# Kernel optimization log

Hardware: AMD Instinct MI355X
Metric: run time of the kernel (lower is better)

Reference implementation:

```python
import jax, jax.numpy as jnp
import numpy as np

EPS = 1e-4

def safe_clamp(x, max_val):
    # nan -> 0, +inf -> max_val, -inf -> -max_val, then clamp to [-max_val, max_val]
    x = jnp.where(jnp.isnan(x), 0.0, x)
    x = jnp.where(jnp.isinf(x) & (x > 0), max_val, x)
    x = jnp.where(jnp.isinf(x) & (x < 0), -max_val, x)
    return jnp.clip(x, -max_val, max_val)

def setup_inputs() -> dict:
    key = jax.random.key(0)
    k1, k2 = jax.random.split(key)
    hidden_states = jax.random.normal(k1, (4, 4096, 2048), dtype=jnp.float32)
    ln_weight = jnp.ones((2048,), dtype=jnp.float32)
    ln_bias = jnp.zeros((2048,), dtype=jnp.float32)
    gate_weight = jax.random.normal(k2, (64, 2048), dtype=jnp.float32) * 0.01
    return {"hidden_states": hidden_states, "ln_weight": ln_weight,
            "ln_bias": ln_bias, "gate_weight": gate_weight}

def reference(hidden_states, ln_weight, ln_bias, gate_weight):
    B, S, H = hidden_states.shape
    top_k = 2
    x = hidden_states.reshape(-1, H)  # (N, H)
    # LayerNorm(eps=1e-5)
    mu = jnp.mean(x, axis=-1, keepdims=True)
    var = jnp.mean((x - mu) ** 2, axis=-1, keepdims=True)
    x = (x - mu) * jax.lax.rsqrt(var + 1e-5) * ln_weight + ln_bias
    x = safe_clamp(x, 50.0)
    # gate: (N, H) @ (H, E)
    router_logits = jnp.clip(x @ gate_weight.T, -10.0, 10.0)
    # eval mode: no noise
    router_probs = jnp.clip(jax.nn.softmax(router_logits, axis=-1), EPS, 1.0)
    top_k_probs, top_k_indices = jax.lax.top_k(router_probs, top_k)
    prob_sum = jnp.maximum(jnp.sum(top_k_probs, axis=-1, keepdims=True), EPS)
    top_k_probs = top_k_probs / prob_sum
    return top_k_probs, top_k_indices, router_logits
```

## Files before the change

### kernel.cpp

```cpp
#include <hip/hip_runtime.h>
#include <math.h>

#define H 2048
#define E 64
#define MR 16
#define NCH 16
#define LR 136

typedef _Float16 half8  __attribute__((ext_vector_type(8)));
typedef _Float16 half4h __attribute__((ext_vector_type(4)));
typedef float    f32x4  __attribute__((ext_vector_type(4)));

#define MFMA16(A,B,C) __builtin_amdgcn_mfma_f32_16x16x32_f16(A,B,C,0,0,0)


__global__ __launch_bounds__(256) void prep_fused(const float* __restrict__ W,
        const float* __restrict__ lnw, const float* __restrict__ lnb,
        _Float16* __restrict__ Bh, _Float16* __restrict__ Bl,
        float* __restrict__ csum, float* __restrict__ bsum) {
    {
        int idx  = blockIdx.x * 256 + threadIdx.x;
        int lane = idx & 63;
        int e  = ((idx >> 6) & 3) * 16 + (lane & 15);
        int k0 = (idx >> 8) * 32 + ((lane >> 4) << 3);
        half8 hh, ll;
        #pragma unroll
        for (int j = 0; j < 8; ++j) {
            float wf = lnw[k0 + j] * W[e * H + k0 + j];
            _Float16 h = (_Float16)wf;
            _Float16 l = (_Float16)((wf - (float)h) * 2048.0f);
            hh[j] = h; ll[j] = l;
        }
        *(half8*)&Bh[(long)idx * 8] = hh;
        *(half8*)&Bl[(long)idx * 8] = ll;
    }
    {
        __shared__ float rc[256], rb[256];
        int e = blockIdx.x, t = threadIdx.x;
        float cs = 0.f, bs = 0.f;
        #pragma unroll
        for (int j = 0; j < 8; ++j) {
            int k = t + j * 256;
            float w = W[e * H + k];
            cs += lnw[k] * w;
            bs += lnb[k] * w;
        }
        rc[t] = cs; rb[t] = bs;
        __syncthreads();
        for (int s = 128; s > 0; s >>= 1) {
            if (t < s) { rc[t] += rc[t + s]; rb[t] += rb[t + s]; }
            __syncthreads();
        }
        if (t == 0) { csum[e] = rc[0]; bsum[e] = rb[0]; }
    }
}

__global__ __launch_bounds__(256, 4) void router_kernel(
    const float* __restrict__ X, const _Float16* __restrict__ Bh,
    const _Float16* __restrict__ Bl, const float* __restrict__ csum,
    const float* __restrict__ bsum, float* __restrict__ out, int nRows)
{
    __shared__ __align__(16) _Float16 Xh[2][MR][LR];
    __shared__ __align__(16) _Float16 Xl[2][MR][LR];
    __shared__ float C2[MR][E + 4];
    __shared__ float mu_s[MR], rs_s[MR];

    const int t    = threadIdx.x;
    const int lane = t & 63;
    const int et   = t >> 6;
    const int q    = lane >> 4;
    const int ln16 = lane & 15;
    const int rowR = t >> 4;
    const int cS   = t & 15;
    const long rowBase = (long)blockIdx.x * MR;
    const long iOff = (long)nRows * 2;
    const long lOff = (long)nRows * 4;

    const float4* Xrow = (const float4*)X + (rowBase + rowR) * 512;

    float sacc = 0.f, qacc = 0.f;

    f32x4 acc0 = (f32x4)0.f;
    f32x4 acc1 = (f32x4)0.f;

    auto convert = [&](const float4* vb, int buf) {
        #pragma unroll
        for (int j = 0; j < 2; ++j) {
            float4 v = vb[j];
            sacc += v.x + v.y + v.z + v.w;
            qacc += v.x * v.x + v.y * v.y + v.z * v.z + v.w * v.w;
            _Float16 h0 = (_Float16)v.x, h1 = (_Float16)v.y,
                     h2 = (_Float16)v.z, h3 = (_Float16)v.w;
            _Float16 l0 = (_Float16)((v.x - (float)h0) * 2048.f);
            _Float16 l1 = (_Float16)((v.y - (float)h1) * 2048.f);
            _Float16 l2 = (_Float16)((v.z - (float)h2) * 2048.f);
            _Float16 l3 = (_Float16)((v.w - (float)h3) * 2048.f);
            half4h hh = {h0, h1, h2, h3};
            half4h ll = {l0, l1, l2, l3};
            int col = (cS + j * 16) * 4;
            *(half4h*)&Xh[buf][rowR][col] = hh;
            *(half4h*)&Xl[buf][rowR][col] = ll;
        }
    };
    auto loadW = [&](half8* Wh, half8* Wl, int c) {
        #pragma unroll
        for (int ks = 0; ks < 4; ++ks) {
            int bo = (((c * 4 + ks) * 4 + et) * 64 + lane) * 8;
            Wh[ks] = *(const half8*)&Bh[bo];
            Wl[ks] = *(const half8*)&Bl[bo];
        }
    };
    auto loadX = [&](float4* vb, int c) {
        #pragma unroll
        for (int j = 0; j < 2; ++j)
            vb[j] = Xrow[c * 32 + cS + j * 16];
    };
    auto mfmaC = [&](const half8* Wh, const half8* Wl, int buf) {
        #pragma unroll
        for (int ks = 0; ks < 4; ++ks) {
            half8 Ah = *(const half8*)&Xh[buf][ln16][ks * 32 + q * 8];
            half8 Al = *(const half8*)&Xl[buf][ln16][ks * 32 + q * 8];
            acc0 = MFMA16(Ah, Wh[ks], acc0);
            acc1 = MFMA16(Ah, Wl[ks], acc1);
            acc1 = MFMA16(Al, Wh[ks], acc1);
        }
    };

    half8 WAh[4], WAl[4], WBh[4], WBl[4];
    float4 vbA[2], vbB[2];

    {
        float4 v0[2];
        loadX(v0, 0);
        loadW(WAh, WAl, 0);
        loadX(vbA, 1);
        convert(v0, 0);
    }
    __syncthreads();

    for (int c = 0; c < NCH; c += 2) {
        loadW(WBh, WBl, c + 1);
        if (c + 2 < NCH) loadX(vbB, c + 2);
        mfmaC(WAh, WAl, 0);
        convert(vbA, 1);
        __syncthreads();

        if (c + 2 < NCH) loadW(WAh, WAl, c + 2);
        if (c + 3 < NCH) loadX(vbA, c + 3);
        mfmaC(WBh, WBl, 1);
        if (c + 2 < NCH) convert(vbB, 0);
        __syncthreads();
    }

    {
        float s = sacc, qq = qacc;
        #pragma unroll
        for (int d = 1; d < 16; d <<= 1) {
            s  += __shfl_xor(s, d);
            qq += __shfl_xor(qq, d);
        }
        if (cS == 0) {
            float mu  = s * (1.f / H);
            float var = qq * (1.f / H) - mu * mu;
            mu_s[rowR] = mu;
            rs_s[rowR] = rsqrtf(var + 1e-5f);
        }
    }
    __syncthreads();

    {
        int n = et * 16 + ln16;
        float cs = csum[n], bs = bsum[n];
        #pragma unroll
        for (int reg = 0; reg < 4; ++reg) {
            int r = q * 4 + reg;
            float raw = acc0[reg] + acc1[reg] * (1.f / 2048.f);
            float lg = rs_s[r] * (raw - mu_s[r] * cs) + bs;
            lg = fminf(fmaxf(lg, -10.f), 10.f);
            out[lOff + (rowBase + r) * 64 + n] = lg;
            C2[r][n] = lg;
        }
    }
    __syncthreads();

    #pragma unroll
    for (int rr = 0; rr < 4; ++rr) {
        int r = et * 4 + rr;
        float l = C2[r][lane];
        float m = l;
        #pragma unroll
        for (int d = 1; d < 64; d <<= 1) m = fmaxf(m, __shfl_xor(m, d));
        float p = __expf(l - m);
        float ssum = p;
        #pragma unroll
        for (int d = 1; d < 64; d <<= 1) ssum += __shfl_xor(ssum, d);
        float prob = fminf(fmaxf(p / ssum, 1e-4f), 1.0f);

        float v1 = prob; int i1 = lane;
        #pragma unroll
        for (int d = 1; d < 64; d <<= 1) {
            float ov = __shfl_xor(v1, d);
            int   oi = __shfl_xor(i1, d);
            if (ov > v1 || (ov == v1 && oi < i1)) { v1 = ov; i1 = oi; }
        }
        float v2 = (lane == i1) ? -1.f : prob; int i2 = lane;
        #pragma unroll
        for (int d = 1; d < 64; d <<= 1) {
            float ov = __shfl_xor(v2, d);
            int   oi = __shfl_xor(i2, d);
            if (ov > v2 || (ov == v2 && oi < i2)) { v2 = ov; i2 = oi; }
        }
        if (lane == 0) {
            float ps = fmaxf(v1 + v2, 1e-4f);
            long rg_ = rowBase + r;
            out[rg_ * 2 + 0] = v1 / ps;
            out[rg_ * 2 + 1] = v2 / ps;
            out[iOff + rg_ * 2 + 0] = (float)i1;
            out[iOff + rg_ * 2 + 1] = (float)i2;
        }
    }
}

extern "C" void kernel_launch(void* const* d_in, const int* in_sizes, int n_in,
                              void* d_out, int out_size, void* d_ws, size_t ws_size,
                              hipStream_t stream) {
    const float* X   = (const float*)d_in[0];
    const float* lnw = (const float*)d_in[1];
    const float* lnb = (const float*)d_in[2];
    const float* W   = (const float*)d_in[3];
    float* outp = (float*)d_out;

    _Float16* Bh = (_Float16*)d_ws;
    _Float16* Bl = Bh + H * E;
    float* csum  = (float*)(Bl + H * E);
    float* bsum  = csum + E;

    int N = in_sizes[0] / H;

    prep_fused<<<64, 256, 0, stream>>>(W, lnw, lnb, Bh, Bl, csum, bsum);
    router_kernel<<<N / MR, 256, 0, stream>>>(X, Bh, Bl, csum, bsum, outp, N);
}
```

Measured before the change: 247.2 us.

## Double chunk size to 256 columns, halving barriers and restructuring W prefetch

Each pipeline stage now covers 256 columns instead of 128, so there are 8 chunks instead of 16 and half as many block barriers. Each thread prefetches four float4 of X per chunk, and the W fragments are loaded just in time in two halves inside each chunk instead of one chunk ahead. This cuts synchronisation overhead. In exchange the LDS buffers are larger, which may lower occupancy, and W load latency is less hidden.

```diff
diff --git a/kernel.cpp b/kernel.cpp
--- a/kernel.cpp
+++ b/kernel.cpp
@@ -4,8 +4,8 @@
 #define H 2048
 #define E 64
 #define MR 16
-#define NCH 16
-#define LR 136
+#define NCH 8
+#define LR 264
 
 typedef _Float16 half8  __attribute__((ext_vector_type(8)));
 typedef _Float16 half4h __attribute__((ext_vector_type(4)));
@@ -79,14 +79,13 @@
     const float4* Xrow = (const float4*)X + (rowBase + rowR) * 512;
 
     float sacc = 0.f, qacc = 0.f;
-
     f32x4 acc0 = (f32x4)0.f;
     f32x4 acc1 = (f32x4)0.f;
 
-    auto convert = [&](const float4* vb, int buf) {
-        #pragma unroll
-        for (int j = 0; j < 2; ++j) {
-            float4 v = vb[j];
+    auto convert = [&](float4 w0, float4 w1, float4 w2, float4 w3, int buf) {
+        #pragma unroll
+        for (int j = 0; j < 4; ++j) {
+            float4 v = (j == 0) ? w0 : (j == 1) ? w1 : (j == 2) ? w2 : w3;
             sacc += v.x + v.y + v.z + v.w;
             qacc += v.x * v.x + v.y * v.y + v.z * v.z + v.w * v.w;
             _Float16 h0 = (_Float16)v.x, h1 = (_Float16)v.y,
@@ -102,53 +101,63 @@
             *(half4h*)&Xl[buf][rowR][col] = ll;
         }
     };
-    auto loadW = [&](half8* Wh, half8* Wl, int c) {
+    auto loadW4 = [&](half8* Wh, half8* Wl, int c, int h) {
         #pragma unroll
         for (int ks = 0; ks < 4; ++ks) {
-            int bo = (((c * 4 + ks) * 4 + et) * 64 + lane) * 8;
+            int gks = c * 8 + h * 4 + ks;
+            int bo = ((gks * 4 + et) * 64 + lane) * 8;
             Wh[ks] = *(const half8*)&Bh[bo];
             Wl[ks] = *(const half8*)&Bl[bo];
         }
     };
-    auto loadX = [&](float4* vb, int c) {
-        #pragma unroll
-        for (int j = 0; j < 2; ++j)
-            vb[j] = Xrow[c * 32 + cS + j * 16];
-    };
-    auto mfmaC = [&](const half8* Wh, const half8* Wl, int buf) {
+    auto mfma4 = [&](const half8* Wh, const half8* Wl, int buf, int h) {
         #pragma unroll
         for (int ks = 0; ks < 4; ++ks) {
-            half8 Ah = *(const half8*)&Xh[buf][ln16][ks * 32 + q * 8];
-            half8 Al = *(const half8*)&Xl[buf][ln16][ks * 32 + q * 8];
+            int col = (h * 4 + ks) * 32 + q * 8;
+            half8 Ah = *(const half8*)&Xh[buf][ln16][col];
+            half8 Al = *(const half8*)&Xl[buf][ln16][col];
             acc0 = MFMA16(Ah, Wh[ks], acc0);
             acc1 = MFMA16(Ah, Wl[ks], acc1);
             acc1 = MFMA16(Al, Wh[ks], acc1);
         }
     };
-
-    half8 WAh[4], WAl[4], WBh[4], WBl[4];
-    float4 vbA[2], vbB[2];
-
-    {
-        float4 v0[2];
-        loadX(v0, 0);
-        loadW(WAh, WAl, 0);
-        loadX(vbA, 1);
-        convert(v0, 0);
+    auto chunkPhase = [&](int c, int buf, bool pf, float4& p0, float4& p1,
+                          float4& p2, float4& p3) {
+        half8 Wh[4], Wl[4];
+        loadW4(Wh, Wl, c, 0);
+        if (pf) {
+            p0 = Xrow[(c + 2) * 64 + cS];
+            p1 = Xrow[(c + 2) * 64 + cS + 16];
+            p2 = Xrow[(c + 2) * 64 + cS + 32];
+            p3 = Xrow[(c + 2) * 64 + cS + 48];
+        }
+        mfma4(Wh, Wl, buf, 0);
+        loadW4(Wh, Wl, c, 1);
+        mfma4(Wh, Wl, buf, 1);
+    };
+
+    float4 vA0, vA1, vA2, vA3, vB0, vB1, vB2, vB3;
+
+    {
+        float4 u0 = Xrow[cS];
+        float4 u1 = Xrow[cS + 16];
+        float4 u2 = Xrow[cS + 32];
+        float4 u3 = Xrow[cS + 48];
+        vA0 = Xrow[64 + cS];
+        vA1 = Xrow[64 + cS + 16];
+        vA2 = Xrow[64 + cS + 32];
+        vA3 = Xrow[64 + cS + 48];
+        convert(u0, u1, u2, u3, 0);
     }
     __syncthreads();
 
     for (int c = 0; c < NCH; c += 2) {
-        loadW(WBh, WBl, c + 1);
-        if (c + 2 < NCH) loadX(vbB, c + 2);
-        mfmaC(WAh, WAl, 0);
-        convert(vbA, 1);
+        chunkPhase(c, 0, c + 2 < NCH, vB0, vB1, vB2, vB3);
+        convert(vA0, vA1, vA2, vA3, 1);
         __syncthreads();
 
-        if (c + 2 < NCH) loadW(WAh, WAl, c + 2);
-        if (c + 3 < NCH) loadX(vbA, c + 3);
-        mfmaC(WBh, WBl, 1);
-        if (c + 2 < NCH) convert(vbB, 0);
+        chunkPhase(c + 1, 1, c + 3 < NCH, vA0, vA1, vA2, vA3);
+        if (c + 2 < NCH) convert(vB0, vB1, vB2, vB3, 0);
         __syncthreads();
     }
 
```

Result: faster. 210.1 us (-15.0%).
